# Optimization experiments

Measured on AMD Instinct MI355X. Metric: run time of the kernel, lower is better.

The kernel has to match this reference:

```python
import jax, jax.numpy as jnp
import numpy as np

DIM = 768
HEADS = 12
HEAD_DIM = DIM // HEADS
SCALE = HEAD_DIM ** -0.5


def setup_inputs() -> dict:
    key = jax.random.key(0)
    k1, k2, k3, k4, k5 = jax.random.split(key, 5)
    B, N = 4, 2048
    x = jax.random.normal(k1, (B, N, DIM), dtype=jnp.float32)
    # qkv Linear: weight [3*dim, dim], bias [3*dim]
    w_qkv = jax.random.normal(k2, (3 * DIM, DIM), dtype=jnp.float32) * (DIM ** -0.5)
    b_qkv = jax.random.normal(k3, (3 * DIM,), dtype=jnp.float32) * 0.01
    # proj Linear: weight [dim, dim], bias [dim]
    w_proj = jax.random.normal(k4, (DIM, DIM), dtype=jnp.float32) * (DIM ** -0.5)
    b_proj = jax.random.normal(k5, (DIM,), dtype=jnp.float32) * 0.01
    return {"x": x, "w_qkv": w_qkv, "b_qkv": b_qkv, "w_proj": w_proj, "b_proj": b_proj}


def reference(x, w_qkv, b_qkv, w_proj, b_proj):
    B, N, C = x.shape
    qkv = (jnp.einsum('bnc,oc->bno', x, w_qkv) + b_qkv)
    qkv = qkv.reshape(B, N, 3, HEADS, HEAD_DIM).transpose(2, 0, 3, 1, 4)
    q, k, v = qkv[0], qkv[1], qkv[2]
    attn = jnp.einsum('bhqd,bhkd->bhqk', q, k) * SCALE
    attn = jax.nn.softmax(attn, axis=-1)
    out = jnp.einsum('bhqk,bhkd->bhqd', attn, v)  # [B, H, N, Dh]
    out = out.transpose(0, 2, 1, 3).reshape(B, N, C)
    # dropout is identity in eval mode
    return jnp.einsum('bnc,oc->bno', out, w_proj) + b_proj
```

## Files before the change

### kernel.cpp

```cpp
#include <hip/hip_runtime.h>
#include <hip/hip_bf16.h>

using bf16 = __hip_bfloat16;
typedef __bf16 bf16x8 __attribute__((ext_vector_type(8)));
typedef short short4v __attribute__((ext_vector_type(4)));
typedef short short8v __attribute__((ext_vector_type(8)));
typedef float float4v __attribute__((ext_vector_type(4)));

#define DIM   768
#define NH    12
#define HD    64
#define SEQ   2048
#define BATCH 4
#define TOK   (BATCH * SEQ)
#define SCALE_QL2E 0.18033688011112042f

#define NX  (TOK * DIM)
#define NWQ (3 * DIM * DIM)
#define NWP (DIM * DIM)

__device__ __forceinline__ short f2bf(float f) {
  union { bf16 h; short s; } u;
  u.h = __float2bfloat16(f);
  return u.s;
}

union frag8 { short4v h[2]; short8v s; bf16x8 b; unsigned u[4]; };

__device__ __forceinline__ void async_copy16(const bf16* g, short* l) {
  __builtin_amdgcn_global_load_lds(
      (const __attribute__((address_space(1))) unsigned int*)g,
      (__attribute__((address_space(3))) unsigned int*)l, 16, 0, 0);
}

#define BARRIER __builtin_amdgcn_s_barrier()
#define LGKM0 asm volatile("s_waitcnt lgkmcnt(0)" ::: "memory")
#define VW0 asm volatile("s_waitcnt vmcnt(0)" ::: "memory")
#define NOSTG (void)0
#define NOVW  (void)0

__global__ void __launch_bounds__(256)
cvt3(const float* __restrict__ a, bf16* __restrict__ oa, long na,
     const float* __restrict__ b, bf16* __restrict__ ob, long nb,
     const float* __restrict__ c, bf16* __restrict__ oc, long nc) {
  const long i = ((long)blockIdx.x * 256 + threadIdx.x) * 8;
  const float* src; bf16* dst; long off;
  if (i < na)                { src = a; dst = oa; off = i; }
  else if (i < na + nb)      { src = b; dst = ob; off = i - na; }
  else if (i < na + nb + nc) { src = c; dst = oc; off = i - na - nb; }
  else return;
  const float4v x0 = *(const float4v*)(src + off);
  const float4v x1 = *(const float4v*)(src + off + 4);
  short8v r;
  r[0] = f2bf(x0[0]); r[1] = f2bf(x0[1]); r[2] = f2bf(x0[2]); r[3] = f2bf(x0[3]);
  r[4] = f2bf(x1[0]); r[5] = f2bf(x1[1]); r[6] = f2bf(x1[2]); r[7] = f2bf(x1[3]);
  *(short8v*)(dst + off) = r;
}

#define STGP(s, p)                                                            \
  async_copy16(pa + (p) * 32,             &As[s][t * 8]);                     \
  async_copy16(pa + 64 * DIM + (p) * 32,  &As[s][2048 + t * 8]);              \
  async_copy16(pb + (p) * 32,             &Bs[s][t * 8]);                     \
  async_copy16(pb + 64 * DIM + (p) * 32,  &Bs[s][2048 + t * 8]);              \
  async_copy16(pb + 128 * DIM + (p) * 32, &Bs[s][4096 + t * 8])

#define PHASE(CUR, STG_, VW_) {                                               \
  bf16x8 af[4], bfv[6];                                                       \
  _Pragma("unroll") for (int mf_ = 0; mf_ < 4; ++mf_)                         \
    af[mf_] = *(const bf16x8*)&As[CUR][mf_ * 512 + arow];                     \
  _Pragma("unroll") for (int nf_ = 0; nf_ < 6; ++nf_)                         \
    bfv[nf_] = *(const bf16x8*)&Bs[CUR][nf_ * 512 + brow];                    \
  STG_; BARRIER; LGKM0;                                                       \
  __builtin_amdgcn_s_setprio(1);                                              \
  _Pragma("unroll") for (int mf_ = 0; mf_ < 4; ++mf_)                         \
  _Pragma("unroll") for (int nf_ = 0; nf_ < 6; ++nf_)                         \
    acc[mf_][nf_] = __builtin_amdgcn_mfma_f32_16x16x32_bf16(                  \
        af[mf_], bfv[nf_], acc[mf_][nf_], 0, 0, 0);                           \
  __builtin_amdgcn_s_setprio(0); VW_; BARRIER; }

__global__ void __launch_bounds__(256, 3)
gemm_qkv(const bf16* __restrict__ X, const bf16* __restrict__ W,
         const float* __restrict__ bias,
         bf16* __restrict__ qb, bf16* __restrict__ kb, bf16* __restrict__ vb) {
  __shared__ short As[2][128 * 32];
  __shared__ short Bs[2][192 * 32];
  const int t = threadIdx.x;
  const int w = t >> 6, l = t & 63, lr = l & 15, q = l >> 4;
  const int wm = w >> 1, wn = w & 1;

  const int orig = blockIdx.x;
  const int swz = (orig & 7) * 96 + (orig >> 3);
  const int tm = swz / 12, tn = swz - tm * 12;
  const int row0 = tm * 128, col0 = tn * 192;

  const int sr = t >> 2;
  const int scol = (((t & 3) << 3) ^ (((sr >> 1) & 3) << 3));
  const bf16* pa  = X + (size_t)(row0 + sr) * DIM + scol;
  const bf16* pb  = W + (size_t)(col0 + sr) * DIM + scol;

  const int acol = ((q << 3) ^ (((lr >> 1) & 3) << 3));
  const int arow = (wm * 64 + lr) * 32 + acol;
  const int brow = (wn * 96 + lr) * 32 + acol;

  float4v acc[4][6] = {};

  STGP(0, 0);
  VW0; BARRIER;

#pragma unroll 1
  for (int k = 0; k < 22; k += 2) {
    PHASE(0, STGP(1, k + 1), VW0)
    PHASE(1, STGP(0, k + 2), VW0)
  }
  PHASE(0, STGP(1, 23), VW0)
  PHASE(1, NOSTG,       NOVW)

#pragma unroll
  for (int nf = 0; nf < 6; ++nf) {
    const int gn = col0 + wn * 96 + nf * 16 + lr;
    const int which = gn / DIM;
    const int cc = gn - which * DIM;
    const int hh = cc >> 6, dd = cc & 63;
    const float bv = bias[gn];
#pragma unroll
    for (int mf = 0; mf < 4; ++mf) {
      const int gm0 = row0 + wm * 64 + mf * 16 + (q << 2);
      const int b = gm0 >> 11, n0 = gm0 & 2047;
      if (which == 2) {
        short4v pv;
#pragma unroll
        for (int r = 0; r < 4; ++r) pv[r] = f2bf(acc[mf][nf][r] + bv);
        *(short4v*)&vb[((size_t)(b * NH + hh) * HD + dd) * SEQ + n0] = pv;
      } else {
        bf16* dst = (which == 0) ? qb : kb;
        const float sc = (which == 0) ? SCALE_QL2E : 1.0f;
#pragma unroll
        for (int r = 0; r < 4; ++r)
          dst[((size_t)(b * NH + hh) * SEQ + n0 + r) * HD + dd] =
              __float2bfloat16((acc[mf][nf][r] + bv) * sc);
      }
    }
  }
}

#define STG_KV(bb, k1)                                                        \
  async_copy16(Kb + (size_t)((k1) + drow) * HD + skey,       &KV[bb][t * 8]); \
  async_copy16(Kb + (size_t)((k1) + 32 + drow) * HD + skey,  &KV[bb][2048 + t * 8]); \
  async_copy16(Vb + (size_t)drow * SEQ + (k1) + skey,        &KV[bb][4096 + t * 8]); \
  async_copy16(Vb + (size_t)(32 + drow) * SEQ + (k1) + skey, &KV[bb][6144 + t * 8])

#define S_STEP(BK_) {                                                         \
  const short* Bf_ = KV[BK_];                                                 \
  __builtin_amdgcn_s_setprio(1);                                              \
  _Pragma("unroll") for (int jn = 0; jn < 4; ++jn) {                          \
    bf16x8 kf[2];                                                             \
    _Pragma("unroll") for (int kq = 0; kq < 2; ++kq)                          \
      kf[kq] = *(const bf16x8*)&Bf_[(jn * 16 + lr) * 64 +                     \
                                    (((kq * 32) + (q << 3)) ^ key8)];         \
    _Pragma("unroll") for (int it = 0; it < 2; ++it)                          \
    _Pragma("unroll") for (int kq = 0; kq < 2; ++kq)                          \
      s[jn][it] = __builtin_amdgcn_mfma_f32_16x16x32_bf16(kf[kq],             \
                      qf[it][kq], s[jn][it], 0, 0, 0);                        \
  }                                                                           \
  __builtin_amdgcn_s_setprio(0); }

#define PV_STEP(PF_, BP_) {                                                   \
  const short* Bv_ = KV[BP_] + 4096;                                          \
  __builtin_amdgcn_s_setprio(1);                                              \
  _Pragma("unroll") for (int c4 = 0; c4 < 2; ++c4) {                          \
    _Pragma("unroll") for (int dj = 0; dj < 4; ++dj) {                        \
      frag8 vf;                                                               \
      vf.h[0] = *(const short4v*)&Bv_[(dj * 16 + lr) * 64 +                   \
                                      ((c4 * 32 + (q << 2)) ^ key8)];         \
      vf.h[1] = *(const short4v*)&Bv_[(dj * 16 + lr) * 64 +                   \
                                      ((c4 * 32 + 16 + (q << 2)) ^ key8)];    \
      _Pragma("unroll") for (int it = 0; it < 2; ++it)                        \
        o[it][dj] = __builtin_amdgcn_mfma_f32_16x16x32_bf16(PF_[c4][it].b,    \
                        vf.b, o[it][dj], 0, 0, 0);                            \
    }                                                                         \
    _Pragma("unroll") for (int it = 0; it < 2; ++it)                          \
      lacc[it] = __builtin_amdgcn_mfma_f32_16x16x32_bf16(PF_[c4][it].b,       \
                     ones.b, lacc[it], 0, 0, 0);                              \
  }                                                                           \
  __builtin_amdgcn_s_setprio(0); }

#define SM_STEP(PF_)                                                          \
  _Pragma("unroll") for (int it = 0; it < 2; ++it)                            \
  _Pragma("unroll") for (int c4 = 0; c4 < 2; ++c4)                            \
  _Pragma("unroll") for (int r = 0; r < 4; ++r) {                             \
    PF_[c4][it].s[r]     = f2bf(__builtin_amdgcn_exp2f(s[2 * c4][it][r]));    \
    PF_[c4][it].s[4 + r] = f2bf(__builtin_amdgcn_exp2f(s[2 * c4 + 1][it][r]));\
  }

#define FA_BODY(BK_, BP_, BN_, PFP_, PFC_, TILE1_) {                          \
  float4v s[4][2] = {};                                                       \
  S_STEP(BK_);                                                                \
  PV_STEP(PFP_, BP_);                                                         \
  STG_KV(BN_, (TILE1_) * 64);                                                 \
  SM_STEP(PFC_);                                                              \
  VW0; BARRIER; }

__global__ void __launch_bounds__(256, 3)
flash_attn(const bf16* __restrict__ Qp, const bf16* __restrict__ Kp,
           const bf16* __restrict__ Vtp, bf16* __restrict__ Op) {
  const int bh = blockIdx.y, qt = blockIdx.x;
  const int t = threadIdx.x, w = t >> 6, l = t & 63, lr = l & 15, q = l >> 4;
  __shared__ short KV[3][8192];

  const bf16* Qb = Qp  + (size_t)(bh * SEQ + qt * 128) * HD;
  const bf16* Kb = Kp  + (size_t)bh * SEQ * HD;
  const bf16* Vb = Vtp + (size_t)bh * HD * SEQ;

  const int drow = t >> 3;
  const int skey = (((t & 7) ^ drow) & 7) * 8;

  bf16x8 qf[2][2];
#pragma unroll
  for (int it = 0; it < 2; ++it)
#pragma unroll
    for (int kq = 0; kq < 2; ++kq)
      qf[it][kq] = *(const bf16x8*)(Qb + (size_t)(w * 32 + it * 16 + lr) * HD +
                                    kq * 32 + q * 8);

  const int key8 = (lr & 7) << 3;

  frag8 ones;
#pragma unroll
  for (int r = 0; r < 8; ++r) ones.s[r] = (short)0x3F80;

  float4v o[2][4] = {};
  float4v lacc[2] = {};
  frag8 pfA[2][2], pfB[2][2];

  STG_KV(0, 0);
  VW0; BARRIER;

  {
    float4v s[4][2] = {};
    S_STEP(0);
    STG_KV(1, 64);
    SM_STEP(pfA);
    VW0; BARRIER;
  }

  int bK = 1;
#pragma unroll 1
  for (int kt = 1; kt < 31; kt += 2) {
    const int bP = (bK == 0) ? 2 : bK - 1;
    const int bN = (bK == 2) ? 0 : bK + 1;
    FA_BODY(bK, bP, bN, pfA, pfB, kt + 1)
    FA_BODY(bN, bK, bP, pfB, pfA, kt + 2)
    bK = bP;
  }

  {
    float4v s[4][2] = {};
    S_STEP(1);
    PV_STEP(pfA, 0);
    SM_STEP(pfB);
    PV_STEP(pfB, 1);
  }

  const int b = bh / NH, h = bh - b * NH;
#pragma unroll
  for (int it = 0; it < 2; ++it)
#pragma unroll
    for (int r = 0; r < 4; ++r) {
      const float linv = 1.0f / lacc[it][r];
      const int grow = b * SEQ + qt * 128 + w * 32 + it * 16 + (q << 2) + r;
      bf16* orow = Op + (size_t)grow * DIM + h * HD;
#pragma unroll
      for (int dj = 0; dj < 4; ++dj)
        orow[dj * 16 + lr] = __float2bfloat16(o[it][dj][r] * linv);
    }
}

#define PRJ_STG(s, p)                                                         \
  async_copy16(pa + (p) * 32,             &Asp[s][t * 8]);                    \
  async_copy16(pb + (p) * 32,             &Bsp[s][t * 8]);                    \
  async_copy16(pb + 64 * DIM + (p) * 32,  &Bsp[s][2048 + t * 8]);             \
  async_copy16(pb + 128 * DIM + (p) * 32, &Bsp[s][4096 + t * 8])

#define PRJ_PHASE(CUR, STG_, VW_) {                                           \
  bf16x8 af[2], bfv[6];                                                       \
  _Pragma("unroll") for (int mf_ = 0; mf_ < 2; ++mf_)                         \
    af[mf_] = *(const bf16x8*)&Asp[CUR][mf_ * 512 + arow];                    \
  _Pragma("unroll") for (int nf_ = 0; nf_ < 6; ++nf_)                         \
    bfv[nf_] = *(const bf16x8*)&Bsp[CUR][nf_ * 512 + brow];                   \
  STG_; BARRIER; LGKM0;                                                       \
  __builtin_amdgcn_s_setprio(1);                                              \
  _Pragma("unroll") for (int mf_ = 0; mf_ < 2; ++mf_)                         \
  _Pragma("unroll") for (int nf_ = 0; nf_ < 6; ++nf_)                         \
    acc[mf_][nf_] = __builtin_amdgcn_mfma_f32_16x16x32_bf16(                  \
        af[mf_], bfv[nf_], acc[mf_][nf_], 0, 0, 0);                           \
  __builtin_amdgcn_s_setprio(0); VW_; BARRIER; }

__global__ void __launch_bounds__(256, 2)
gemm_proj(const bf16* __restrict__ A, const bf16* __restrict__ W,
          const float* __restrict__ bias, float* __restrict__ out) {
  __shared__ short Asp[2][64 * 32];
  __shared__ short Bsp[2][192 * 32];
  const int t = threadIdx.x;
  const int w = t >> 6, l = t & 63, lr = l & 15, q = l >> 4;
  const int wm = w >> 1, wn = w & 1;

  const int orig = blockIdx.x;
  const int swz = (orig & 7) * 64 + (orig >> 3);
  const int tm = swz >> 2, tn = swz & 3;
  const int row0 = tm * 64, col0 = tn * 192;

  const int sr = t >> 2;
  const int scol = (((t & 3) << 3) ^ (((sr >> 1) & 3) << 3));
  const bf16* pa = A + (size_t)(row0 + sr) * DIM + scol;
  const bf16* pb = W + (size_t)(col0 + sr) * DIM + scol;

  const int acol = ((q << 3) ^ (((lr >> 1) & 3) << 3));
  const int arow = (wm * 32 + lr) * 32 + acol;
  const int brow = (wn * 96 + lr) * 32 + acol;

  float4v acc[2][6] = {};

  PRJ_STG(0, 0);
  VW0; BARRIER;

#pragma unroll 1
  for (int k = 0; k < 22; k += 2) {
    PRJ_PHASE(0, PRJ_STG(1, k + 1), VW0)
    PRJ_PHASE(1, PRJ_STG(0, k + 2), VW0)
  }
  PRJ_PHASE(0, PRJ_STG(1, 23), VW0)
  PRJ_PHASE(1, NOSTG,          NOVW)

#pragma unroll
  for (int nf = 0; nf < 6; ++nf) {
    const int gn = col0 + wn * 96 + nf * 16 + lr;
    const float bv = bias[gn];
#pragma unroll
    for (int mf = 0; mf < 2; ++mf) {
#pragma unroll
      for (int r = 0; r < 4; ++r) {
        const int gm = row0 + wm * 32 + mf * 16 + (q << 2) + r;
        out[(size_t)gm * DIM + gn] = acc[mf][nf][r] + bv;
      }
    }
  }
}

extern "C" void kernel_launch(void* const* d_in, const int* in_sizes, int n_in,
                              void* d_out, int out_size, void* d_ws, size_t ws_size,
                              hipStream_t stream) {
  const float* x      = (const float*)d_in[0];
  const float* w_qkv  = (const float*)d_in[1];
  const float* b_qkv  = (const float*)d_in[2];
  const float* w_proj = (const float*)d_in[3];
  const float* b_proj = (const float*)d_in[4];
  float* out = (float*)d_out;

  const size_t perbuf = (size_t)BATCH * NH * SEQ * HD;
  bf16* qb  = (bf16*)d_ws;
  bf16* kb  = qb + perbuf;
  bf16* vb  = kb + perbuf;
  bf16* ao  = vb + perbuf;
  bf16* xb  = ao + perbuf;
  bf16* wqb = xb + (size_t)NX;
  bf16* wpb = wqb + (size_t)NWQ;

  const int cvt_blocks = (NX + NWQ + NWP) / 8 / 256;
  cvt3<<<cvt_blocks, 256, 0, stream>>>(x, xb, NX, w_qkv, wqb, NWQ, w_proj, wpb, NWP);
  gemm_qkv <<<dim3(768), 256, 0, stream>>>(xb, wqb, b_qkv, qb, kb, vb);
  flash_attn<<<dim3(SEQ / 128, BATCH * NH), 256, 0, stream>>>(qb, kb, vb, ao);
  gemm_proj <<<dim3(512), 256, 0, stream>>>(ao, wpb, b_proj, out);
}
```

Baseline: 198.5 us.

## Replace LDS double-buffered QKV GEMM with direct global-to-register MFMA loads

Removes the shared-memory staging, async copies, barriers and double-buffer pipeline from the QKV projection GEMM, and instead loads A and B fragments straight from global memory into registers for each MFMA. This removes LDS traffic and synchronisation overhead. In exchange, tiles are no longer shared across waves, so global/L2 traffic rises, loads use a strided per-lane pattern, and there is no explicit prefetch to hide memory latency.

```diff
diff --git a/kernel.cpp b/kernel.cpp
--- a/kernel.cpp
+++ b/kernel.cpp
@@ -57,33 +57,10 @@
   *(short8v*)(dst + off) = r;
 }
 
-#define STGP(s, p)                                                            \
-  async_copy16(pa + (p) * 32,             &As[s][t * 8]);                     \
-  async_copy16(pa + 64 * DIM + (p) * 32,  &As[s][2048 + t * 8]);              \
-  async_copy16(pb + (p) * 32,             &Bs[s][t * 8]);                     \
-  async_copy16(pb + 64 * DIM + (p) * 32,  &Bs[s][2048 + t * 8]);              \
-  async_copy16(pb + 128 * DIM + (p) * 32, &Bs[s][4096 + t * 8])
-
-#define PHASE(CUR, STG_, VW_) {                                               \
-  bf16x8 af[4], bfv[6];                                                       \
-  _Pragma("unroll") for (int mf_ = 0; mf_ < 4; ++mf_)                         \
-    af[mf_] = *(const bf16x8*)&As[CUR][mf_ * 512 + arow];                     \
-  _Pragma("unroll") for (int nf_ = 0; nf_ < 6; ++nf_)                         \
-    bfv[nf_] = *(const bf16x8*)&Bs[CUR][nf_ * 512 + brow];                    \
-  STG_; BARRIER; LGKM0;                                                       \
-  __builtin_amdgcn_s_setprio(1);                                              \
-  _Pragma("unroll") for (int mf_ = 0; mf_ < 4; ++mf_)                         \
-  _Pragma("unroll") for (int nf_ = 0; nf_ < 6; ++nf_)                         \
-    acc[mf_][nf_] = __builtin_amdgcn_mfma_f32_16x16x32_bf16(                  \
-        af[mf_], bfv[nf_], acc[mf_][nf_], 0, 0, 0);                           \
-  __builtin_amdgcn_s_setprio(0); VW_; BARRIER; }
-
 __global__ void __launch_bounds__(256, 3)
 gemm_qkv(const bf16* __restrict__ X, const bf16* __restrict__ W,
          const float* __restrict__ bias,
          bf16* __restrict__ qb, bf16* __restrict__ kb, bf16* __restrict__ vb) {
-  __shared__ short As[2][128 * 32];
-  __shared__ short Bs[2][192 * 32];
   const int t = threadIdx.x;
   const int w = t >> 6, l = t & 63, lr = l & 15, q = l >> 4;
   const int wm = w >> 1, wn = w & 1;
@@ -93,27 +70,26 @@
   const int tm = swz / 12, tn = swz - tm * 12;
   const int row0 = tm * 128, col0 = tn * 192;
 
-  const int sr = t >> 2;
-  const int scol = (((t & 3) << 3) ^ (((sr >> 1) & 3) << 3));
-  const bf16* pa  = X + (size_t)(row0 + sr) * DIM + scol;
-  const bf16* pb  = W + (size_t)(col0 + sr) * DIM + scol;
-
-  const int acol = ((q << 3) ^ (((lr >> 1) & 3) << 3));
-  const int arow = (wm * 64 + lr) * 32 + acol;
-  const int brow = (wn * 96 + lr) * 32 + acol;
+  const bf16* Ab = X + (size_t)(row0 + wm * 64 + lr) * DIM + q * 8;
+  const bf16* Bb = W + (size_t)(col0 + wn * 96 + lr) * DIM + q * 8;
 
   float4v acc[4][6] = {};
 
-  STGP(0, 0);
-  VW0; BARRIER;
-
-#pragma unroll 1
-  for (int k = 0; k < 22; k += 2) {
-    PHASE(0, STGP(1, k + 1), VW0)
-    PHASE(1, STGP(0, k + 2), VW0)
-  }
-  PHASE(0, STGP(1, 23), VW0)
-  PHASE(1, NOSTG,       NOVW)
+#pragma unroll 2
+  for (int k0 = 0; k0 < DIM; k0 += 32) {
+    bf16x8 af[4];
+#pragma unroll
+    for (int mf = 0; mf < 4; ++mf)
+      af[mf] = *(const bf16x8*)(Ab + (size_t)(mf * 16) * DIM + k0);
+#pragma unroll
+    for (int nf = 0; nf < 6; ++nf) {
+      const bf16x8 bfv = *(const bf16x8*)(Bb + (size_t)(nf * 16) * DIM + k0);
+#pragma unroll
+      for (int mf = 0; mf < 4; ++mf)
+        acc[mf][nf] = __builtin_amdgcn_mfma_f32_16x16x32_bf16(af[mf], bfv,
+                                                              acc[mf][nf], 0, 0, 0);
+    }
+  }
 
 #pragma unroll
   for (int nf = 0; nf < 6; ++nf) {
```

New measurement: 246.3 us. 1.24x slower.
